# Performance work log

Hardware: AMD Instinct MI355X
Metric: run time of the kernel (lower is better)

Reference implementation:

```python
import jax, jax.numpy as jnp
import numpy as np

B, V, L, C = 4, 8, 256, 1024
H, O = 16, 4
Dh = C // H
NEG = -1e9

def setup_inputs() -> dict:
    key = jax.random.key(0)
    ks = jax.random.split(key, 16)
    inp = {}
    inp['v'] = jax.random.normal(ks[0], (B, V, L, C), jnp.float32)
    inp['k'] = jax.random.normal(ks[1], (B, V, L, C), jnp.float32)
    inp['q'] = jax.random.normal(ks[2], (B, V, L, C), jnp.float32)
    inp['masks'] = jax.random.uniform(ks[3], (O, B, V, 1, 1, L)) < 0.15  # True = masked out
    inp['tau'] = jnp.ones((1,), jnp.float32)
    inp['training'] = 1
    u = jax.random.uniform(ks[4], (B, V, O), jnp.float32, minval=1e-20, maxval=1.0)
    inp['gumbel_noise'] = -jnp.log(-jnp.log(u))  # standard Gumbel, = -log(Exp(1))
    s = 1.0 / np.sqrt(C)
    inp['Wv'] = jax.random.normal(ks[5], (C, C), jnp.float32) * s
    inp['bv'] = jnp.zeros((C,), jnp.float32)
    inp['Wk'] = jax.random.normal(ks[6], (C, C), jnp.float32) * s
    inp['bk'] = jnp.zeros((C,), jnp.float32)
    inp['Wq'] = jax.random.normal(ks[7], (C, C), jnp.float32) * s
    inp['bq'] = jnp.zeros((C,), jnp.float32)
    inp['Wm'] = jax.random.normal(ks[8], (C, C), jnp.float32) * s
    inp['bm'] = jnp.zeros((C,), jnp.float32)
    inp['W1'] = jax.random.normal(ks[9], (C, C // 2), jnp.float32) * s
    inp['W2'] = jax.random.normal(ks[10], (C // 2, O), jnp.float32) * (1.0 / np.sqrt(C // 2))
    inp['b2'] = jnp.zeros((O,), jnp.float32)
    return inp


def reference(v, k, q, masks, tau, training, gumbel_noise,
              Wv, bv, Wk, bk, Wq, bq, Wm, bm, W1, W2, b2):
    # --- HardRoutingBlock (pooling='avg'): avg-pool over seq, MLP, gumbel-softmax ---
    pooled = jnp.mean(v, axis=2)                          # [B,V,C]
    h = jax.nn.relu(pooled @ W1)                          # [B,V,C/2]
    logits = h @ W2 + b2                                  # [B,V,O]
    logp = jax.nn.log_softmax(logits, axis=-1)
    alphas = jax.nn.softmax((logp + gumbel_noise) / tau[0], axis=-1)  # [B,V,O]

    # --- multi-head projections: [B,V,L,C] -> [B,V,H,L,Dh] ---
    def split_heads(x):
        return x.reshape(B, V, L, H, Dh).transpose(0, 1, 3, 2, 4)
    vv = split_heads(v @ Wv + bv)
    kk = split_heads(k @ Wk + bk)
    qq = split_heads(q @ Wq + bq)

    scores = jnp.einsum('bvhqd,bvhkd->bvhqk', qq, kk) / np.sqrt(Dh)  # [B,V,H,L,L]
    # per-order masked softmax: masks [O,B,V,1,1,L]
    att = jax.nn.softmax(jnp.where(masks, NEG, scores[None]), axis=-1)  # [O,B,V,H,L,L]
    # routed combination: einsum('bvl,bvlcnm->bvcnm') with l=orders
    att_map = jnp.einsum('bvo,obvhqk->bvhqk', alphas, att)
    atted = jnp.einsum('bvhqk,bvhkd->bvhqd', att_map, vv)  # [B,V,H,L,Dh]
    atted = atted.transpose(0, 1, 3, 2, 4).reshape(B, V, L, C)
    return atted @ Wm + bm
```

## Files before the change

kernel.cpp:

```cpp
#include <hip/hip_runtime.h>

#define B_   4
#define V_   8
#define L_   256
#define C_   1024
#define H_   16
#define O_   4
#define DH_  64
#define BV_  32
#define M_   8192
#define MB_  (1024 * 1024)

typedef short bf16x8 __attribute__((ext_vector_type(8)));
typedef short bf16x4 __attribute__((ext_vector_type(4)));
typedef float f32x4  __attribute__((ext_vector_type(4)));
typedef float f32x16 __attribute__((ext_vector_type(16)));

__device__ __forceinline__ float bflo(unsigned int w) { return __uint_as_float(w << 16); }
__device__ __forceinline__ float bfhi(unsigned int w) { return __uint_as_float(w & 0xffff0000u); }
__device__ __forceinline__ unsigned int f2bfbits(float f) {
    unsigned int i = __float_as_uint(f);
    return (i + 0x7fffu + ((i >> 16) & 1u)) >> 16;
}
__device__ __forceinline__ unsigned int packbf(float a, float b) {
    return f2bfbits(a) | (f2bfbits(b) << 16);
}
__device__ __forceinline__ unsigned int cvtpk_bf16(float lo, float hi) {
    unsigned int r;
    asm("v_cvt_pk_bf16_f32 %0, %1, %2" : "=v"(r) : "v"(lo), "v"(hi));
    return r;
}

typedef const __attribute__((address_space(1))) unsigned int* gas_t;
typedef __attribute__((address_space(3))) unsigned int* las_t;
__device__ __forceinline__ void gll16(const void* g, void* l) {
    __builtin_amdgcn_global_load_lds((gas_t)g, (las_t)l, 16, 0, 0);
}

__device__ __forceinline__ void conv_body(const float* __restrict__ in,
                                          unsigned short* __restrict__ outp,
                                          int blk, int t)
{
    const size_t i = ((size_t)blk * 256 + t) * 8;
    const float4 f0 = *(const float4*)(in + i);
    const float4 f1 = *(const float4*)(in + i + 4);
    uint4 o;
    o.x = packbf(f0.x, f0.y); o.y = packbf(f0.z, f0.w);
    o.z = packbf(f1.x, f1.y); o.w = packbf(f1.z, f1.w);
    *(uint4*)(outp + i) = o;
}

__device__ __forceinline__ void pools_body(const float* __restrict__ v,
                                           float* __restrict__ pbuf2,
                                           int pb, int t)
{
    const int bv = pb >> 3, lc = pb & 7;
    const float* vb = v + (size_t)bv * (L_ * C_) + (size_t)lc * 32 * C_ + t * 4;
    float a0 = 0.f, a1 = 0.f, a2 = 0.f, a3 = 0.f;
#pragma unroll
    for (int l = 0; l < 32; ++l) {
        const float4 f = *(const float4*)(vb + (size_t)l * C_);
        a0 += f.x; a1 += f.y; a2 += f.z; a3 += f.w;
    }
    float4 o; o.x = a0; o.y = a1; o.z = a2; o.w = a3;
    *(float4*)(pbuf2 + ((size_t)lc * 32 + bv) * C_ + t * 4) = o;
}

__device__ __forceinline__ void wprep_body(const float* __restrict__ W,
                                           unsigned short* __restrict__ Wt,
                                           float (*tile)[65], int k0, int n0, int t)
{
    const int r = t >> 2, c4 = (t & 3) * 16;
#pragma unroll
    for (int i = 0; i < 4; ++i) {
        const float4 f = *(const float4*)(W + (size_t)(k0 + r) * C_ + n0 + c4 + i * 4);
        tile[r][c4 + i * 4 + 0] = f.x; tile[r][c4 + i * 4 + 1] = f.y;
        tile[r][c4 + i * 4 + 2] = f.z; tile[r][c4 + i * 4 + 3] = f.w;
    }
    __syncthreads();
    unsigned int ow[8];
#pragma unroll
    for (int p = 0; p < 8; ++p)
        ow[p] = packbf(tile[c4 + 2 * p][r], tile[c4 + 2 * p + 1][r]);
    unsigned short* dst = Wt + (size_t)(n0 + r) * C_ + k0 + c4;
    uint4 o0; o0.x = ow[0]; o0.y = ow[1]; o0.z = ow[2]; o0.w = ow[3];
    uint4 o1; o1.x = ow[4]; o1.y = ow[5]; o1.z = ow[6]; o1.w = ow[7];
    *(uint4*)dst = o0;
    *(uint4*)(dst + 8) = o1;
}

__global__ __launch_bounds__(256) void conv_k(const float* __restrict__ in,
                                              unsigned short* __restrict__ outp)
{ conv_body(in, outp, blockIdx.x, threadIdx.x); }

__global__ __launch_bounds__(256) void pools_k(const float* __restrict__ v,
                                               float* __restrict__ pbuf2)
{ pools_body(v, pbuf2, blockIdx.x, threadIdx.x); }

__global__ __launch_bounds__(256) void wprep_k(const float* __restrict__ W,
                                               unsigned short* __restrict__ Wt)
{
    __shared__ float tile[64][65];
    wprep_body(W, Wt, tile, blockIdx.x * 64, blockIdx.y * 64, threadIdx.x);
}

__global__ __launch_bounds__(1024) void maskpack_k(
    const void* __restrict__ src, unsigned char* __restrict__ dst)
{
    __shared__ int v_word;
    const int t = threadIdx.x;
    if (t == 0) v_word = 1;
    __syncthreads();
    const unsigned int* s32 = (const unsigned int*)src;
    const unsigned int w = s32[t];
    if (w > 1u && w != 0x3F800000u) atomicAnd(&v_word, 0);
    __syncthreads();
    const bool word_mode = (v_word != 0);
    const unsigned char* s8 = (const unsigned char*)src;
#pragma unroll
    for (int i = 0; i < 8; ++i) {
        const int idx = t * 8 + i;
        const int bv = idx >> 8, l = idx & 255;
        unsigned int bits = 0;
#pragma unroll
        for (int o = 0; o < O_; ++o) {
            const int mi = (o * BV_ + bv) * L_ + l;
            const unsigned int m = word_mode ? (s32[mi] != 0u) : (s8[mi] != 0);
            bits |= m << o;
        }
        dst[idx] = (unsigned char)bits;
    }
}

__global__ __launch_bounds__(256) void prep_k(
    const float* __restrict__ q, const float* __restrict__ k, const float* __restrict__ v,
    const void* __restrict__ msk,
    const float* __restrict__ Wq, const float* __restrict__ Wk,
    const float* __restrict__ Wv, const float* __restrict__ Wm,
    unsigned short* __restrict__ cq, unsigned short* __restrict__ ck,
    unsigned short* __restrict__ cv,
    float* __restrict__ pbuf2, unsigned char* __restrict__ mpk,
    unsigned short* __restrict__ Wtb)
{
    __shared__ float tile[64][65];
    const int blk = blockIdx.x;
    const int t = threadIdx.x;
    if (blk < 12288) {
        const int wsel = blk >> 12;
        const float* in = (wsel == 0) ? q : (wsel == 1) ? k : v;
        unsigned short* outp = (wsel == 0) ? cq : (wsel == 1) ? ck : cv;
        conv_body(in, outp, blk & 4095, t);
    } else if (blk < 12544) {
        pools_body(v, pbuf2, blk - 12288, t);
    } else if (blk < 12548) {
        __shared__ int v_word;
        if (t == 0) v_word = 1;
        __syncthreads();
        const unsigned int* s32 = (const unsigned int*)msk;
        const unsigned int w = s32[t];
        if (w > 1u && w != 0x3F800000u) atomicAnd(&v_word, 0);
        __syncthreads();
        const bool word_mode = (v_word != 0);
        const unsigned char* s8 = (const unsigned char*)msk;
        const int tt = (blk - 12544) * 256 + t;
#pragma unroll
        for (int i = 0; i < 8; ++i) {
            const int idx = tt * 8 + i;
            const int bv = idx >> 8, l = idx & 255;
            unsigned int bits = 0;
#pragma unroll
            for (int o = 0; o < O_; ++o) {
                const int mi = (o * BV_ + bv) * L_ + l;
                const unsigned int m = word_mode ? (s32[mi] != 0u) : (s8[mi] != 0);
                bits |= m << o;
            }
            mpk[idx] = (unsigned char)bits;
        }
    } else {
        const int wb = blk - 12548;
        const int wsel = wb >> 8;
        const float* W = (wsel == 0) ? Wq : (wsel == 1) ? Wk : (wsel == 2) ? Wv : Wm;
        unsigned short* Wt = Wtb + (size_t)wsel * (C_ * C_);
        const int b = wb & 255;
        wprep_body(W, Wt, tile, (b & 15) * 64, (b >> 4) * 64, t);
    }
}

__global__ __launch_bounds__(256) void poolr_k(const float* __restrict__ pbuf2,
                                               float* __restrict__ pooled)
{
    const int idx = blockIdx.x * 256 + threadIdx.x;
    float s = 0.f;
#pragma unroll
    for (int p = 0; p < 8; ++p) s += pbuf2[(size_t)p * (32 * C_) + idx];
    pooled[idx] = s * (1.0f / 256.0f);
}

__global__ __launch_bounds__(256) void mlp1_k(const float* __restrict__ pooled,
                                              const float* __restrict__ W1,
                                              float* __restrict__ pbuf)
{
    const int t = threadIdx.x;
    const int col = blockIdx.x * 32 + (t & 31);
    const int b0 = (t >> 5) * 4;
    const int c0 = blockIdx.y * 32;
    float a0 = 0.f, a1 = 0.f, a2 = 0.f, a3 = 0.f;
#pragma unroll
    for (int c = c0; c < c0 + 32; ++c) {
        const float wv = W1[(size_t)c * 512 + col];
        a0 = fmaf(pooled[(size_t)(b0 + 0) * C_ + c], wv, a0);
        a1 = fmaf(pooled[(size_t)(b0 + 1) * C_ + c], wv, a1);
        a2 = fmaf(pooled[(size_t)(b0 + 2) * C_ + c], wv, a2);
        a3 = fmaf(pooled[(size_t)(b0 + 3) * C_ + c], wv, a3);
    }
    const size_t pb = ((size_t)blockIdx.y * 32 + b0) * 512 + col;
    pbuf[pb]        = a0;
    pbuf[pb + 512]  = a1;
    pbuf[pb + 1024] = a2;
    pbuf[pb + 1536] = a3;
}

__global__ __launch_bounds__(256) void mlp2_k(const float* __restrict__ pbuf,
                                              const float* __restrict__ W2,
                                              const float* __restrict__ b2,
                                              const float* __restrict__ gum,
                                              const float* __restrict__ tau,
                                              float* __restrict__ alphas)
{
    __shared__ float red[4][O_];
    const int bv = blockIdx.x, t = threadIdx.x;
    float h0 = 0.f, h1 = 0.f;
#pragma unroll
    for (int ch = 0; ch < 32; ++ch) {
        h0 += pbuf[((size_t)ch * 32 + bv) * 512 + t];
        h1 += pbuf[((size_t)ch * 32 + bv) * 512 + 256 + t];
    }
    h0 = fmaxf(h0, 0.f); h1 = fmaxf(h1, 0.f);
    float part[O_];
#pragma unroll
    for (int o = 0; o < O_; ++o)
        part[o] = h0 * W2[t * O_ + o] + h1 * W2[(t + 256) * O_ + o];
#pragma unroll
    for (int off = 32; off >= 1; off >>= 1) {
#pragma unroll
        for (int o = 0; o < O_; ++o) part[o] += __shfl_down(part[o], off, 64);
    }
    const int wid = t >> 6, lane = t & 63;
    if (lane == 0) {
#pragma unroll
        for (int o = 0; o < O_; ++o) red[wid][o] = part[o];
    }
    __syncthreads();
    if (t == 0) {
        float lg[O_];
#pragma unroll
        for (int o = 0; o < O_; ++o)
            lg[o] = red[0][o] + red[1][o] + red[2][o] + red[3][o] + b2[o];
        float mx = fmaxf(fmaxf(lg[0], lg[1]), fmaxf(lg[2], lg[3]));
        float s = 0.f;
#pragma unroll
        for (int o = 0; o < O_; ++o) s += expf(lg[o] - mx);
        const float lse = logf(s) + mx;
        const float it = 1.0f / tau[0];
        float y[O_];
#pragma unroll
        for (int o = 0; o < O_; ++o) y[o] = (lg[o] - lse + gum[bv * O_ + o]) * it;
        float my = fmaxf(fmaxf(y[0], y[1]), fmaxf(y[2], y[3]));
        float z = 0.f;
#pragma unroll
        for (int o = 0; o < O_; ++o) { y[o] = expf(y[o] - my); z += y[o]; }
        const float iz = 1.0f / z;
#pragma unroll
        for (int o = 0; o < O_; ++o) alphas[bv * O_ + o] = y[o] * iz;
    }
}

template <bool PROJSTORE>
__device__ __forceinline__ void mgemm_body(
    const unsigned short* __restrict__ Ab, const unsigned short* __restrict__ Wt,
    const float* __restrict__ bias, void* __restrict__ out_, int n0, int m0)
{
    __shared__ unsigned short As[128][64];
    __shared__ unsigned short Bs[128][64];
    const int t = threadIdx.x;
    const int w = t >> 6, lane = t & 63;
    const int wm = (w >> 1) * 64, wn = (w & 1) * 64;
    const int fr = lane & 15;
    const int fq = lane >> 4;

    const int sr = w * 8 + (lane >> 3);
    const int sc = ((lane & 7) ^ ((lane >> 3) & 7)) * 8;
    const unsigned short* aP = Ab + (size_t)(m0 + sr) * C_ + sc;
    const unsigned short* bP = Wt + (size_t)(n0 + sr) * C_ + sc;

    const int frm = (fr & 7);

    f32x4 acc[4][4] = {};

    for (int kt = 0; kt < C_; kt += 64) {
        __syncthreads();
#pragma unroll
        for (int i = 0; i < 4; ++i) {
            gll16(aP + (size_t)i * 32 * C_ + kt, &As[i * 32 + w * 8][0]);
            gll16(bP + (size_t)i * 32 * C_ + kt, &Bs[i * 32 + w * 8][0]);
        }
        __syncthreads();

#pragma unroll
        for (int c = 0; c < 2; ++c) {
            const int rk = ((c * 4 + fq) ^ frm) * 8;
            bf16x8 af[4], bfr[4];
#pragma unroll
            for (int i = 0; i < 4; ++i)
                af[i] = *(const bf16x8*)&As[wm + i * 16 + fr][rk];
#pragma unroll
            for (int j = 0; j < 4; ++j)
                bfr[j] = *(const bf16x8*)&Bs[wn + j * 16 + fr][rk];
#pragma unroll
            for (int i = 0; i < 4; ++i)
#pragma unroll
                for (int j = 0; j < 4; ++j)
                    acc[i][j] = __builtin_amdgcn_mfma_f32_16x16x32_bf16(af[i], bfr[j], acc[i][j], 0, 0, 0);
        }
    }

#pragma unroll
    for (int j = 0; j < 4; ++j) {
        const int gcol = n0 + wn + j * 16 + fr;
        const float bj = bias[gcol];
#pragma unroll
        for (int i = 0; i < 4; ++i) {
#pragma unroll
            for (int r = 0; r < 4; ++r) {
                const int grow = m0 + wm + i * 16 + fq * 4 + r;
                const float val = acc[i][j][r] + bj;
                if (PROJSTORE) {
                    const int bvb = grow >> 8, l = grow & 255;
                    const int hh = gcol >> 6, dh = gcol & 63;
                    ((unsigned short*)out_)[(((size_t)bvb * H_ + hh) * L_ + l) * DH_ + dh] =
                        (unsigned short)f2bfbits(val);
                } else {
                    ((float*)out_)[(size_t)grow * C_ + gcol] = val;
                }
            }
        }
    }
}

template <bool PROJSTORE>
__global__ __launch_bounds__(256) void mgemm_k(
    const unsigned short* __restrict__ Ab, const unsigned short* __restrict__ Wt,
    const float* __restrict__ bias, void* __restrict__ out_)
{
    mgemm_body<PROJSTORE>(Ab, Wt, bias, out_, blockIdx.x * 128, blockIdx.y * 128);
}

__global__ __launch_bounds__(256) void mgemm3_k(
    const unsigned short* __restrict__ cq, const unsigned short* __restrict__ ck,
    const unsigned short* __restrict__ cv, const unsigned short* __restrict__ Wtb,
    const float* __restrict__ bq, const float* __restrict__ bk, const float* __restrict__ bvv,
    unsigned short* __restrict__ qqw, unsigned short* __restrict__ kkw,
    unsigned short* __restrict__ vvw)
{
    const int b = blockIdx.x;
    const int swz = (b & 7) * 192 + (b >> 3);
    const int which = swz >> 9;
    const int g = swz & 511;
    const unsigned short* A = (which == 0) ? cq : (which == 1) ? ck : cv;
    const unsigned short* W = Wtb + (size_t)which * (C_ * C_);
    const float* bias = (which == 0) ? bq : (which == 1) ? bk : bvv;
    unsigned short* outp = (which == 0) ? qqw : (which == 1) ? kkw : vvw;
    mgemm_body<true>(A, W, bias, (void*)outp, (g & 7) * 128, (g >> 3) * 128);
}

__global__ __launch_bounds__(256) void mgemmf_k(
    const unsigned short* __restrict__ Ab, const unsigned short* __restrict__ Wt,
    const float* __restrict__ bias, float* __restrict__ out_)
{
    const int b = blockIdx.x;
    const int swz = (b & 7) * 64 + (b >> 3);
    mgemm_body<false>(Ab, Wt, bias, (void*)out_, (swz & 7) * 128, (swz >> 3) * 128);
}

__global__ __launch_bounds__(256) void attn_t_k(
    const unsigned short* __restrict__ qq, const unsigned short* __restrict__ kk,
    const unsigned char* __restrict__ mpk, const float* __restrict__ alphas,
    float* __restrict__ cbuf)
{
    __shared__ unsigned int mkw[64];
    __shared__ float al[O_];
    const int h = blockIdx.x, bv = blockIdx.y;
    const int t = threadIdx.x;
    const int w = t >> 6, lane = t & 63;
    const int fr = lane & 31, hf = lane >> 5;
    const size_t hb = ((size_t)bv * H_ + h) * (L_ * DH_);

    if (t < 64) mkw[t] = ((const unsigned int*)mpk)[bv * 64 + t];
    if (t < O_) al[t] = alphas[bv * O_ + t];
    __syncthreads();
    const float al0 = al[0], al1 = al[1], al2 = al[2], al3 = al[3];

#pragma unroll 1
    for (int qt = 0; qt < 2; ++qt) {
        const int q32 = w * 64 + qt * 32;
        bf16x8 qf[4];
#pragma unroll
        for (int st = 0; st < 4; ++st)
            qf[st] = *(const bf16x8*)(qq + hb + (size_t)(q32 + fr) * DH_ + st * 16 + hf * 8);

        float T0 = 0.f, T1 = 0.f, T2 = 0.f, T3 = 0.f;
#pragma unroll 1
        for (int j = 0; j < 8; ++j) {
            bf16x8 kf[4];
#pragma unroll
            for (int st = 0; st < 4; ++st)
                kf[st] = *(const bf16x8*)(kk + hb + (size_t)(j * 32 + fr) * DH_ + st * 16 + hf * 8);
            f32x16 s = {};
#pragma unroll
            for (int st = 0; st < 4; ++st)
                s = __builtin_amdgcn_mfma_f32_32x32x16_bf16(kf[st], qf[st], s, 0, 0, 0);
#pragma unroll
            for (int c = 0; c < 4; ++c) {
                const unsigned int iv = (~mkw[j * 8 + c * 2 + hf]) & 0x0F0F0F0Fu;
#pragma unroll
                for (int r = 0; r < 4; ++r) {
                    const float e = __expf(s[c * 4 + r] * 0.125f);
                    const unsigned int nib = iv >> (r * 8);
                    T0 = fmaf(e, (float)( nib       & 1u), T0);
                    T1 = fmaf(e, (float)((nib >> 1) & 1u), T1);
                    T2 = fmaf(e, (float)((nib >> 2) & 1u), T2);
                    T3 = fmaf(e, (float)((nib >> 3) & 1u), T3);
                }
            }
        }
        T0 += __shfl_xor(T0, 32, 64);
        T1 += __shfl_xor(T1, 32, 64);
        T2 += __shfl_xor(T2, 32, 64);
        T3 += __shfl_xor(T3, 32, 64);
        if (hf == 0) {
            float4 cv;
            cv.x = al0 * __builtin_amdgcn_rcpf(fmaxf(T0, 1e-30f));
            cv.y = al1 * __builtin_amdgcn_rcpf(fmaxf(T1, 1e-30f));
            cv.z = al2 * __builtin_amdgcn_rcpf(fmaxf(T2, 1e-30f));
            cv.w = al3 * __builtin_amdgcn_rcpf(fmaxf(T3, 1e-30f));
            *(float4*)(cbuf + (((size_t)bv * H_ + h) * L_ + q32 + fr) * 4) = cv;
        }
    }
}

__global__ __launch_bounds__(256) void attn_pv_k(
    const unsigned short* __restrict__ qq, const unsigned short* __restrict__ kk,
    const unsigned short* __restrict__ vv, const unsigned char* __restrict__ mpk,
    const float* __restrict__ cbuf, unsigned short* __restrict__ atted)
{
    __shared__ unsigned short Vt[DH_][260];
    __shared__ unsigned int mkw[64];
    const int h = blockIdx.x, bv = blockIdx.y;
    const int t = threadIdx.x;
    const int w = t >> 6, lane = t & 63;
    const int fr = lane & 31, hf = lane >> 5;
    const size_t hb = ((size_t)bv * H_ + h) * (L_ * DH_);

    {
        const uint4* gv = (const uint4*)(vv + hb + (size_t)t * DH_);
#pragma unroll
        for (int i = 0; i < 8; ++i) {
            const uint4 wv = gv[i];
            const unsigned int ws4[4] = {wv.x, wv.y, wv.z, wv.w};
#pragma unroll
            for (int jd = 0; jd < 4; ++jd) {
                Vt[i * 8 + jd * 2 + 0][t] = (unsigned short)(ws4[jd] & 0xffffu);
                Vt[i * 8 + jd * 2 + 1][t] = (unsigned short)(ws4[jd] >> 16);
            }
        }
    }
    if (t < 64) mkw[t] = ((const unsigned int*)mpk)[bv * 64 + t];
    __syncthreads();

#pragma unroll 1
    for (int qt = 0; qt < 2; ++qt) {
        const int q32 = w * 64 + qt * 32;
        bf16x8 qf[4];
#pragma unroll
        for (int st = 0; st < 4; ++st)
            qf[st] = *(const bf16x8*)(qq + hb + (size_t)(q32 + fr) * DH_ + st * 16 + hf * 8);
        const float4 cv = *(const float4*)(cbuf + (((size_t)bv * H_ + h) * L_ + q32 + fr) * 4);
        const float c0 = cv.x, c1 = cv.y, c2 = cv.z, c3 = cv.w;

        f32x16 o0 = {};
        f32x16 o1 = {};
#pragma unroll 1
        for (int j = 0; j < 8; ++j) {
            bf16x8 kf[4];
#pragma unroll
            for (int st = 0; st < 4; ++st)
                kf[st] = *(const bf16x8*)(kk + hb + (size_t)(j * 32 + fr) * DH_ + st * 16 + hf * 8);
            f32x16 s = {};
#pragma unroll
            for (int st = 0; st < 4; ++st)
                s = __builtin_amdgcn_mfma_f32_32x32x16_bf16(kf[st], qf[st], s, 0, 0, 0);

            unsigned int pe[4][2];
#pragma unroll
            for (int c = 0; c < 4; ++c) {
                const unsigned int iv = (~mkw[j * 8 + c * 2 + hf]) & 0x0F0F0F0Fu;
                float p[4];
#pragma unroll
                for (int r = 0; r < 4; ++r) {
                    const float e = __expf(s[c * 4 + r] * 0.125f);
                    const unsigned int nib = iv >> (r * 8);
                    float cf =      c0 * (float)( nib       & 1u);
                    cf = fmaf(c1, (float)((nib >> 1) & 1u), cf);
                    cf = fmaf(c2, (float)((nib >> 2) & 1u), cf);
                    cf = fmaf(c3, (float)((nib >> 3) & 1u), cf);
                    p[r] = e * cf;
                }
                pe[c][0] = cvtpk_bf16(p[0], p[1]);
                pe[c][1] = cvtpk_bf16(p[2], p[3]);
            }
#pragma unroll
            for (int b = 0; b < 2; ++b) {
                const unsigned int qe0 = pe[2 * b][0],     qe1 = pe[2 * b][1];
                const unsigned int qo0 = pe[2 * b + 1][0], qo1 = pe[2 * b + 1][1];
                const unsigned int xe0 = (unsigned int)__shfl_xor((int)qe0, 32, 64);
                const unsigned int xe1 = (unsigned int)__shfl_xor((int)qe1, 32, 64);
                const unsigned int xo0 = (unsigned int)__shfl_xor((int)qo0, 32, 64);
                const unsigned int xo1 = (unsigned int)__shfl_xor((int)qo1, 32, 64);
                union { unsigned int d[4]; bf16x8 v; } pa;
                pa.d[0] = hf ? xo0 : qe0;
                pa.d[1] = hf ? xo1 : qe1;
                pa.d[2] = hf ? qo0 : xe0;
                pa.d[3] = hf ? qo1 : xe1;

                const int kc = j * 32 + b * 16 + hf * 8;
                union { struct { bf16x4 lo, hi; } p2; bf16x8 v; } v0u, v1u;
                v0u.p2.lo = *(const bf16x4*)&Vt[ 0 + fr][kc];
                v0u.p2.hi = *(const bf16x4*)&Vt[ 0 + fr][kc + 4];
                v1u.p2.lo = *(const bf16x4*)&Vt[32 + fr][kc];
                v1u.p2.hi = *(const bf16x4*)&Vt[32 + fr][kc + 4];
                o0 = __builtin_amdgcn_mfma_f32_32x32x16_bf16(pa.v, v0u.v, o0, 0, 0, 0);
                o1 = __builtin_amdgcn_mfma_f32_32x32x16_bf16(pa.v, v1u.v, o1, 0, 0, 0);
            }
        }
#pragma unroll
        for (int reg = 0; reg < 16; ++reg) {
            const int qrow = q32 + (reg & 3) + 8 * (reg >> 2) + 4 * hf;
            unsigned short* dst = atted + ((size_t)bv * L_ + qrow) * C_ + h * DH_;
            dst[fr]      = (unsigned short)f2bfbits(o0[reg]);
            dst[32 + fr] = (unsigned short)f2bfbits(o1[reg]);
        }
    }
}

extern "C" void kernel_launch(void* const* d_in, const int* in_sizes, int n_in,
                              void* d_out, int out_size, void* d_ws, size_t ws_size,
                              hipStream_t stream)
{
    (void)in_sizes; (void)n_in; (void)out_size;
    const float* v   = (const float*)d_in[0];
    const float* k   = (const float*)d_in[1];
    const float* q   = (const float*)d_in[2];
    const void*  msk = d_in[3];
    const float* tau = (const float*)d_in[4];
    const float* gum = (const float*)d_in[6];
    const float* Wv  = (const float*)d_in[7];
    const float* bvp = (const float*)d_in[8];
    const float* Wk  = (const float*)d_in[9];
    const float* bkp = (const float*)d_in[10];
    const float* Wq  = (const float*)d_in[11];
    const float* bqp = (const float*)d_in[12];
    const float* Wm  = (const float*)d_in[13];
    const float* bmp = (const float*)d_in[14];
    const float* W1  = (const float*)d_in[15];
    const float* W2  = (const float*)d_in[16];
    const float* b2  = (const float*)d_in[17];
    float* out = (float*)d_out;

    char* ws = (char*)d_ws;

    if (ws_size >= (size_t)128 * MB_) {
        float* alphas       = (float*)ws;
        unsigned char* mpk  = (unsigned char*)(ws + 1024);
        float* pooled       = (float*)(ws + 16384);
        float* pbuf2        = (float*)(ws + 147456);
        float* pbuf         = (float*)(ws + 1196032);
        unsigned short* Wtb = (unsigned short*)(ws + (size_t)4 * MB_);
        float* cbuf         = (float*)(ws + (size_t)12 * MB_);
        unsigned short* cq  = (unsigned short*)(ws + (size_t)14 * MB_);
        unsigned short* ck  = (unsigned short*)(ws + (size_t)30 * MB_);
        unsigned short* cv  = (unsigned short*)(ws + (size_t)46 * MB_);
        unsigned short* qqw = (unsigned short*)(ws + (size_t)62 * MB_);
        unsigned short* kkw = (unsigned short*)(ws + (size_t)78 * MB_);
        unsigned short* vvw = (unsigned short*)(ws + (size_t)94 * MB_);
        unsigned short* atw = (unsigned short*)(ws + (size_t)110 * MB_);

        hipLaunchKernelGGL(prep_k, dim3(13572), dim3(256), 0, stream,
                           q, k, v, msk, Wq, Wk, Wv, Wm, cq, ck, cv, pbuf2, mpk, Wtb);
        hipLaunchKernelGGL(poolr_k, dim3(128), dim3(256), 0, stream, pbuf2, pooled);
        hipLaunchKernelGGL(mlp1_k, dim3(16, 32), dim3(256), 0, stream, pooled, W1, pbuf);
        hipLaunchKernelGGL(mlp2_k, dim3(BV_), dim3(256), 0, stream,
                           pbuf, W2, b2, gum, tau, alphas);
        hipLaunchKernelGGL(mgemm3_k, dim3(1536), dim3(256), 0, stream,
                           cq, ck, cv, Wtb, bqp, bkp, bvp, qqw, kkw, vvw);
        hipLaunchKernelGGL(attn_t_k, dim3(H_, BV_), dim3(256), 0, stream,
                           qqw, kkw, mpk, alphas, cbuf);
        hipLaunchKernelGGL(attn_pv_k, dim3(H_, BV_), dim3(256), 0, stream,
                           qqw, kkw, vvw, mpk, cbuf, atw);
        hipLaunchKernelGGL(mgemmf_k, dim3(512), dim3(256), 0, stream,
                           atw, Wtb + (size_t)3 * (C_ * C_), bmp, out);
    } else {
        float* alphas       = (float*)ws;
        unsigned char* mpk  = (unsigned char*)(ws + 1024);
        float* pooled       = (float*)(ws + 16384);
        float* pbuf2        = (float*)(ws + 147456);
        float* pbuf         = (float*)(ws + 1196032);
        unsigned short* Wt  = (unsigned short*)(ws + 16384);
        float* cbuf         = (float*)(ws + 16384);
        unsigned short* qqw = (unsigned short*)(ws + 2113536);
        unsigned short* kkw = qqw + (size_t)M_ * C_;
        unsigned short* vvw = kkw + (size_t)M_ * C_;
        unsigned short* atw = vvw + (size_t)M_ * C_;

        hipLaunchKernelGGL(pools_k, dim3(256), dim3(256), 0, stream, v, pbuf2);
        hipLaunchKernelGGL(poolr_k, dim3(128), dim3(256), 0, stream, pbuf2, pooled);
        hipLaunchKernelGGL(mlp1_k, dim3(16, 32), dim3(256), 0, stream, pooled, W1, pbuf);
        hipLaunchKernelGGL(mlp2_k, dim3(BV_), dim3(256), 0, stream,
                           pbuf, W2, b2, gum, tau, alphas);
        hipLaunchKernelGGL(maskpack_k, dim3(1), dim3(1024), 0, stream, msk, mpk);

        hipLaunchKernelGGL(conv_k, dim3(4096), dim3(256), 0, stream, q, atw);
        hipLaunchKernelGGL(wprep_k, dim3(16, 16), dim3(256), 0, stream, Wq, Wt);
        hipLaunchKernelGGL((mgemm_k<true>), dim3(8, 64), dim3(256), 0, stream,
                           atw, Wt, bqp, (void*)qqw);
        hipLaunchKernelGGL(conv_k, dim3(4096), dim3(256), 0, stream, k, atw);
        hipLaunchKernelGGL(wprep_k, dim3(16, 16), dim3(256), 0, stream, Wk, Wt);
        hipLaunchKernelGGL((mgemm_k<true>), dim3(8, 64), dim3(256), 0, stream,
                           atw, Wt, bkp, (void*)kkw);
        hipLaunchKernelGGL(conv_k, dim3(4096), dim3(256), 0, stream, v, atw);
        hipLaunchKernelGGL(wprep_k, dim3(16, 16), dim3(256), 0, stream, Wv, Wt);
        hipLaunchKernelGGL((mgemm_k<true>), dim3(8, 64), dim3(256), 0, stream,
                           atw, Wt, bvp, (void*)vvw);

        hipLaunchKernelGGL(attn_t_k, dim3(H_, BV_), dim3(256), 0, stream,
                           qqw, kkw, mpk, alphas, cbuf);
        hipLaunchKernelGGL(attn_pv_k, dim3(H_, BV_), dim3(256), 0, stream,
                           qqw, kkw, vvw, mpk, cbuf, atw);

        hipLaunchKernelGGL(wprep_k, dim3(16, 16), dim3(256), 0, stream, Wm, Wt);
        hipLaunchKernelGGL((mgemm_k<false>), dim3(8, 64), dim3(256), 0, stream,
                           atw, Wt, bmp, (void*)out);
    }
}
```

Measured before the change: 187.9 us.

## Fuse fp32-to-bf16 conversion of q/k/v into projection GEMM A-tile loads

Removes the separate conversion pass that wrote bf16 copies of q, k and v. The projection GEMM now loads fp32 A directly into registers, packs it to bf16 and stores it swizzled into shared memory, while B still uses global_load_lds. This cuts one full fp32 read plus a bf16 write and re-read of three 32 MB tensors, and lowers the workspace requirement. In exchange the A path goes through registers and explicit LDS stores instead of direct-to-LDS loads, which can raise register pressure and reduce load/compute overlap in the GEMM's inner loop.

```diff
diff --git a/kernel.cpp b/kernel.cpp
--- a/kernel.cpp
+++ b/kernel.cpp
@@ -37,19 +37,6 @@
     __builtin_amdgcn_global_load_lds((gas_t)g, (las_t)l, 16, 0, 0);
 }
 
-__device__ __forceinline__ void conv_body(const float* __restrict__ in,
-                                          unsigned short* __restrict__ outp,
-                                          int blk, int t)
-{
-    const size_t i = ((size_t)blk * 256 + t) * 8;
-    const float4 f0 = *(const float4*)(in + i);
-    const float4 f1 = *(const float4*)(in + i + 4);
-    uint4 o;
-    o.x = packbf(f0.x, f0.y); o.y = packbf(f0.z, f0.w);
-    o.z = packbf(f1.x, f1.y); o.w = packbf(f1.z, f1.w);
-    *(uint4*)(outp + i) = o;
-}
-
 __device__ __forceinline__ void pools_body(const float* __restrict__ v,
                                            float* __restrict__ pbuf2,
                                            int pb, int t)
@@ -88,10 +75,6 @@
     *(uint4*)dst = o0;
     *(uint4*)(dst + 8) = o1;
 }
-
-__global__ __launch_bounds__(256) void conv_k(const float* __restrict__ in,
-                                              unsigned short* __restrict__ outp)
-{ conv_body(in, outp, blockIdx.x, threadIdx.x); }
 
 __global__ __launch_bounds__(256) void pools_k(const float* __restrict__ v,
                                                float* __restrict__ pbuf2)
@@ -133,26 +116,18 @@
 }
 
 __global__ __launch_bounds__(256) void prep_k(
-    const float* __restrict__ q, const float* __restrict__ k, const float* __restrict__ v,
-    const void* __restrict__ msk,
+    const float* __restrict__ v, const void* __restrict__ msk,
     const float* __restrict__ Wq, const float* __restrict__ Wk,
     const float* __restrict__ Wv, const float* __restrict__ Wm,
-    unsigned short* __restrict__ cq, unsigned short* __restrict__ ck,
-    unsigned short* __restrict__ cv,
     float* __restrict__ pbuf2, unsigned char* __restrict__ mpk,
     unsigned short* __restrict__ Wtb)
 {
     __shared__ float tile[64][65];
     const int blk = blockIdx.x;
     const int t = threadIdx.x;
-    if (blk < 12288) {
-        const int wsel = blk >> 12;
-        const float* in = (wsel == 0) ? q : (wsel == 1) ? k : v;
-        unsigned short* outp = (wsel == 0) ? cq : (wsel == 1) ? ck : cv;
-        conv_body(in, outp, blk & 4095, t);
-    } else if (blk < 12544) {
-        pools_body(v, pbuf2, blk - 12288, t);
-    } else if (blk < 12548) {
+    if (blk < 256) {
+        pools_body(v, pbuf2, blk, t);
+    } else if (blk < 260) {
         __shared__ int v_word;
         if (t == 0) v_word = 1;
         __syncthreads();
@@ -162,7 +137,7 @@
         __syncthreads();
         const bool word_mode = (v_word != 0);
         const unsigned char* s8 = (const unsigned char*)msk;
-        const int tt = (blk - 12544) * 256 + t;
+        const int tt = (blk - 256) * 256 + t;
 #pragma unroll
         for (int i = 0; i < 8; ++i) {
             const int idx = tt * 8 + i;
@@ -177,7 +152,7 @@
             mpk[idx] = (unsigned char)bits;
         }
     } else {
-        const int wb = blk - 12548;
+        const int wb = blk - 260;
         const int wsel = wb >> 8;
         const float* W = (wsel == 0) ? Wq : (wsel == 1) ? Wk : (wsel == 2) ? Wv : Wm;
         unsigned short* Wt = Wtb + (size_t)wsel * (C_ * C_);
@@ -275,9 +250,9 @@
     }
 }
 
-template <bool PROJSTORE>
+template <bool AF32, bool PROJSTORE>
 __device__ __forceinline__ void mgemm_body(
-    const unsigned short* __restrict__ Ab, const unsigned short* __restrict__ Wt,
+    const void* __restrict__ A_, const unsigned short* __restrict__ Wt,
     const float* __restrict__ bias, void* __restrict__ out_, int n0, int m0)
 {
     __shared__ unsigned short As[128][64];
@@ -289,21 +264,47 @@
     const int fq = lane >> 4;
 
     const int sr = w * 8 + (lane >> 3);
-    const int sc = ((lane & 7) ^ ((lane >> 3) & 7)) * 8;
-    const unsigned short* aP = Ab + (size_t)(m0 + sr) * C_ + sc;
-    const unsigned short* bP = Wt + (size_t)(n0 + sr) * C_ + sc;
+    const int sl = lane & 7;
+    const int xk = (lane >> 3) & 7;
+    const int scp = (sl ^ xk) * 8;
+
+    const unsigned short* bP = Wt + (size_t)(n0 + sr) * C_ + scp;
+    const float* aF = (const float*)A_ + (size_t)(m0 + sr) * C_ + sl * 8;
+    const unsigned short* aH = (const unsigned short*)A_ + (size_t)(m0 + sr) * C_ + scp;
 
     const int frm = (fr & 7);
 
     f32x4 acc[4][4] = {};
 
     for (int kt = 0; kt < C_; kt += 64) {
+        float4 av[4][2];
+        if (AF32) {
+#pragma unroll
+            for (int i = 0; i < 4; ++i) {
+                const float* p = aF + (size_t)i * 32 * C_ + kt;
+                av[i][0] = *(const float4*)p;
+                av[i][1] = *(const float4*)(p + 4);
+            }
+        }
         __syncthreads();
-#pragma unroll
-        for (int i = 0; i < 4; ++i) {
-            gll16(aP + (size_t)i * 32 * C_ + kt, &As[i * 32 + w * 8][0]);
+        if (AF32) {
+#pragma unroll
+            for (int i = 0; i < 4; ++i) {
+                uint4 o;
+                o.x = packbf(av[i][0].x, av[i][0].y);
+                o.y = packbf(av[i][0].z, av[i][0].w);
+                o.z = packbf(av[i][1].x, av[i][1].y);
+                o.w = packbf(av[i][1].z, av[i][1].w);
+                *(uint4*)&As[i * 32 + sr][scp] = o;
+            }
+        } else {
+#pragma unroll
+            for (int i = 0; i < 4; ++i)
+                gll16(aH + (size_t)i * 32 * C_ + kt, &As[i * 32 + w * 8][0]);
+        }
+#pragma unroll
+        for (int i = 0; i < 4; ++i)
             gll16(bP + (size_t)i * 32 * C_ + kt, &Bs[i * 32 + w * 8][0]);
-        }
         __syncthreads();
 
 #pragma unroll
@@ -347,17 +348,17 @@
     }
 }
 
-template <bool PROJSTORE>
+template <bool AF32, bool PROJSTORE>
 __global__ __launch_bounds__(256) void mgemm_k(
-    const unsigned short* __restrict__ Ab, const unsigned short* __restrict__ Wt,
+    const void* __restrict__ A_, const unsigned short* __restrict__ Wt,
     const float* __restrict__ bias, void* __restrict__ out_)
 {
-    mgemm_body<PROJSTORE>(Ab, Wt, bias, out_, blockIdx.x * 128, blockIdx.y * 128);
+    mgemm_body<AF32, PROJSTORE>(A_, Wt, bias, out_, blockIdx.x * 128, blockIdx.y * 128);
 }
 
 __global__ __launch_bounds__(256) void mgemm3_k(
-    const unsigned short* __restrict__ cq, const unsigned short* __restrict__ ck,
-    const unsigned short* __restrict__ cv, const unsigned short* __restrict__ Wtb,
+    const float* __restrict__ q, const float* __restrict__ k,
+    const float* __restrict__ v, const unsigned short* __restrict__ Wtb,
     const float* __restrict__ bq, const float* __restrict__ bk, const float* __restrict__ bvv,
     unsigned short* __restrict__ qqw, unsigned short* __restrict__ kkw,
     unsigned short* __restrict__ vvw)
@@ -366,11 +367,11 @@
     const int swz = (b & 7) * 192 + (b >> 3);
     const int which = swz >> 9;
     const int g = swz & 511;
-    const unsigned short* A = (which == 0) ? cq : (which == 1) ? ck : cv;
+    const float* A = (which == 0) ? q : (which == 1) ? k : v;
     const unsigned short* W = Wtb + (size_t)which * (C_ * C_);
     const float* bias = (which == 0) ? bq : (which == 1) ? bk : bvv;
     unsigned short* outp = (which == 0) ? qqw : (which == 1) ? kkw : vvw;
-    mgemm_body<true>(A, W, bias, (void*)outp, (g & 7) * 128, (g >> 3) * 128);
+    mgemm_body<true, true>((const void*)A, W, bias, (void*)outp, (g & 7) * 128, (g >> 3) * 128);
 }
 
 __global__ __launch_bounds__(256) void mgemmf_k(
@@ -379,7 +380,8 @@
 {
     const int b = blockIdx.x;
     const int swz = (b & 7) * 64 + (b >> 3);
-    mgemm_body<false>(Ab, Wt, bias, (void*)out_, (swz & 7) * 128, (swz >> 3) * 128);
+    mgemm_body<false, false>((const void*)Ab, Wt, bias, (void*)out_,
+                             (swz & 7) * 128, (swz >> 3) * 128);
 }
 
 __global__ __launch_bounds__(256) void attn_t_k(
@@ -578,7 +580,7 @@
 
     char* ws = (char*)d_ws;
 
-    if (ws_size >= (size_t)128 * MB_) {
+    if (ws_size >= (size_t)80 * MB_) {
         float* alphas       = (float*)ws;
         unsigned char* mpk  = (unsigned char*)(ws + 1024);
         float* pooled       = (float*)(ws + 16384);
@@ -586,22 +588,19 @@
         float* pbuf         = (float*)(ws + 1196032);
         unsigned short* Wtb = (unsigned short*)(ws + (size_t)4 * MB_);
         float* cbuf         = (float*)(ws + (size_t)12 * MB_);
-        unsigned short* cq  = (unsigned short*)(ws + (size_t)14 * MB_);
-        unsigned short* ck  = (unsigned short*)(ws + (size_t)30 * MB_);
-        unsigned short* cv  = (unsigned short*)(ws + (size_t)46 * MB_);
-        unsigned short* qqw = (unsigned short*)(ws + (size_t)62 * MB_);
-        unsigned short* kkw = (unsigned short*)(ws + (size_t)78 * MB_);
-        unsigned short* vvw = (unsigned short*)(ws + (size_t)94 * MB_);
-        unsigned short* atw = (unsigned short*)(ws + (size_t)110 * MB_);
-
-        hipLaunchKernelGGL(prep_k, dim3(13572), dim3(256), 0, stream,
-                           q, k, v, msk, Wq, Wk, Wv, Wm, cq, ck, cv, pbuf2, mpk, Wtb);
+        unsigned short* qqw = (unsigned short*)(ws + (size_t)14 * MB_);
+        unsigned short* kkw = (unsigned short*)(ws + (size_t)30 * MB_);
+        unsigned short* vvw = (unsigned short*)(ws + (size_t)46 * MB_);
+        unsigned short* atw = (unsigned short*)(ws + (size_t)62 * MB_);
+
+        hipLaunchKernelGGL(prep_k, dim3(1284), dim3(256), 0, stream,
+                           v, msk, Wq, Wk, Wv, Wm, pbuf2, mpk, Wtb);
         hipLaunchKernelGGL(poolr_k, dim3(128), dim3(256), 0, stream, pbuf2, pooled);
         hipLaunchKernelGGL(mlp1_k, dim3(16, 32), dim3(256), 0, stream, pooled, W1, pbuf);
         hipLaunchKernelGGL(mlp2_k, dim3(BV_), dim3(256), 0, stream,
                            pbuf, W2, b2, gum, tau, alphas);
         hipLaunchKernelGGL(mgemm3_k, dim3(1536), dim3(256), 0, stream,
-                           cq, ck, cv, Wtb, bqp, bkp, bvp, qqw, kkw, vvw);
+                           q, k, v, Wtb, bqp, bkp, bvp, qqw, kkw, vvw);
         hipLaunchKernelGGL(attn_t_k, dim3(H_, BV_), dim3(256), 0, stream,
                            qqw, kkw, mpk, alphas, cbuf);
         hipLaunchKernelGGL(attn_pv_k, dim3(H_, BV_), dim3(256), 0, stream,
@@ -628,18 +627,15 @@
                            pbuf, W2, b2, gum, tau, alphas);
         hipLaunchKernelGGL(maskpack_k, dim3(1), dim3(1024), 0, stream, msk, mpk);
 
-        hipLaunchKernelGGL(conv_k, dim3(4096), dim3(256), 0, stream, q, atw);
         hipLaunchKernelGGL(wprep_k, dim3(16, 16), dim3(256), 0, stream, Wq, Wt);
-        hipLaunchKernelGGL((mgemm_k<true>), dim3(8, 64), dim3(256), 0, stream,
-                           atw, Wt, bqp, (void*)qqw);
-        hipLaunchKernelGGL(conv_k, dim3(4096), dim3(256), 0, stream, k, atw);
+        hipLaunchKernelGGL((mgemm_k<true, true>), dim3(8, 64), dim3(256), 0, stream,
+                           (const void*)q, Wt, bqp, (void*)qqw);
         hipLaunchKernelGGL(wprep_k, dim3(16, 16), dim3(256), 0, stream, Wk, Wt);
-        hipLaunchKernelGGL((mgemm_k<true>), dim3(8, 64), dim3(256), 0, stream,
-                           atw, Wt, bkp, (void*)kkw);
-        hipLaunchKernelGGL(conv_k, dim3(4096), dim3(256), 0, stream, v, atw);
+        hipLaunchKernelGGL((mgemm_k<true, true>), dim3(8, 64), dim3(256), 0, stream,
+                           (const void*)k, Wt, bkp, (void*)kkw);
         hipLaunchKernelGGL(wprep_k, dim3(16, 16), dim3(256), 0, stream, Wv, Wt);
-        hipLaunchKernelGGL((mgemm_k<true>), dim3(8, 64), dim3(256), 0, stream,
-                           atw, Wt, bvp, (void*)vvw);
+        hipLaunchKernelGGL((mgemm_k<true, true>), dim3(8, 64), dim3(256), 0, stream,
+                           (const void*)v, Wt, bvp, (void*)vvw);
 
         hipLaunchKernelGGL(attn_t_k, dim3(H_, BV_), dim3(256), 0, stream,
                            qqw, kkw, mpk, alphas, cbuf);
@@ -647,7 +643,7 @@
                            qqw, kkw, vvw, mpk, cbuf, atw);
 
         hipLaunchKernelGGL(wprep_k, dim3(16, 16), dim3(256), 0, stream, Wm, Wt);
-        hipLaunchKernelGGL((mgemm_k<false>), dim3(8, 64), dim3(256), 0, stream,
-                           atw, Wt, bmp, (void*)out);
-    }
-}
+        hipLaunchKernelGGL((mgemm_k<false, false>), dim3(8, 64), dim3(256), 0, stream,
+                           (const void*)atw, Wt, bmp, (void*)out);
+    }
+}
```

Result: no change. 190.5 us (+1.4%).
